# Kernel optimization log

Hardware: AMD Instinct MI355X
Metric: run time of the kernel (lower is better)

## Reference

```python
import jax, jax.numpy as jnp
import numpy as np

IMAGE_SIZE = 800
OUT = 50          # feature map size
FEAT = 512
SCALES = (2.0, 4.0, 6.0)
RATIOS = (0.5, 1.0, 1.5)
A = len(SCALES) * len(RATIOS)          # 9 anchors per cell
POS_THR, NEG_THR = 0.7, 0.3
W_CONF, W_REG = 1.0, 5.0
SCALE = IMAGE_SIZE // OUT              # 16, stride of feature map


def _anchor_base():
    # order: ratio outer loop, scale inner loop (matches get_anchor_base)
    ws = jnp.array([s * r for r in RATIOS for s in SCALES], jnp.float32)  # [A]
    hs = jnp.array([s for r in RATIOS for s in SCALES], jnp.float32)      # [A]
    cx = (jnp.arange(OUT, dtype=jnp.float32) + 0.5)[:, None, None]        # grid dim0 -> x
    cy = (jnp.arange(OUT, dtype=jnp.float32) + 0.5)[None, :, None]        # grid dim1 -> y
    xmin = jnp.clip(cx - ws / 2, 0.0, OUT)
    xmax = jnp.clip(cx + ws / 2, 0.0, OUT)
    ymin = jnp.clip(cy - hs / 2, 0.0, OUT)
    ymax = jnp.clip(cy + hs / 2, 0.0, OUT)
    shp = (OUT, OUT, A)
    base = jnp.stack([jnp.broadcast_to(xmin, shp), jnp.broadcast_to(ymin, shp),
                      jnp.broadcast_to(xmax, shp), jnp.broadcast_to(ymax, shp)], axis=-1)
    return base.reshape(-1, 4)         # [N,4], N = OUT*OUT*A = 22500


def _iou(anchors, gt):
    # anchors [N,4], gt [B,M,4] (xyxy) -> iou [B,N,M]
    a = anchors[None, :, None, :]
    g = gt[:, None, :, :]
    ix1 = jnp.maximum(a[..., 0], g[..., 0]); iy1 = jnp.maximum(a[..., 1], g[..., 1])
    ix2 = jnp.minimum(a[..., 2], g[..., 2]); iy2 = jnp.minimum(a[..., 3], g[..., 3])
    inter = jnp.clip(ix2 - ix1, 0.0) * jnp.clip(iy2 - iy1, 0.0)
    area_a = (a[..., 2] - a[..., 0]) * (a[..., 3] - a[..., 1])
    area_g = (g[..., 2] - g[..., 0]) * (g[..., 3] - g[..., 1])
    return inter / (area_a + area_g - inter + 1e-8)


def _smooth_l1(d):
    ad = jnp.abs(d)
    return jnp.where(ad < 1.0, 0.5 * d * d, ad - 0.5)


def setup_inputs() -> dict:
    key = jax.random.key(0)
    ks = jax.random.split(key, 8)
    B, M = 16, 16
    features = jax.random.normal(ks[0], (B, FEAT, OUT, OUT), jnp.float32)
    # valid GT boxes in image coords: centers in [100,700], sizes in [32,200]
    cxy = jax.random.uniform(ks[1], (B, M, 2), jnp.float32, 100.0, 700.0)
    wh = jax.random.uniform(ks[2], (B, M, 2), jnp.float32, 32.0, 200.0)
    x1y1 = jnp.clip(cxy - wh / 2, 0.0, IMAGE_SIZE)
    x2y2 = jnp.clip(cxy + wh / 2, 0.0, IMAGE_SIZE)
    gt_boxes = jnp.concatenate([x1y1, x2y2], axis=-1)
    w1 = jax.random.normal(ks[3], (FEAT, FEAT, 3, 3), jnp.float32) * 0.02
    b1 = jnp.zeros((FEAT,), jnp.float32)
    w_cls = jax.random.normal(ks[4], (A, FEAT), jnp.float32) * 0.02
    b_cls = jnp.zeros((A,), jnp.float32)
    w_box = jax.random.normal(ks[5], (4 * A, FEAT), jnp.float32) * 0.02
    b_box = jnp.zeros((4 * A,), jnp.float32)
    return {"features": features, "gt_boxes": gt_boxes, "w1": w1, "b1": b1,
            "w_cls": w_cls, "b_cls": b_cls, "w_box": w_box, "b_box": b_box}


def reference(features, gt_boxes, w1, b1, w_cls, b_cls, w_box, b_box):
    B = features.shape[0]
    anchors = _anchor_base()                                   # [N,4]
    N = anchors.shape[0]

    # --- conv tower ---
    x = jax.lax.conv_general_dilated(features, w1, (1, 1), 'SAME') + b1[None, :, None, None]
    cls_map = jnp.einsum('bchw,ac->bahw', x, w_cls) + b_cls[None, :, None, None]   # [B,A,H,W]
    box_map = jnp.einsum('bchw,dc->bdhw', x, w_box) + b_box[None, :, None, None]   # [B,4A,H,W]
    logits = jnp.transpose(cls_map, (0, 2, 3, 1)).reshape(B, N)                    # [B,N]
    pred_off = jnp.transpose(box_map.reshape(B, A, 4, OUT, OUT), (0, 3, 4, 1, 2)).reshape(B, N, 4)

    # --- project gt to feature-map (anchor) coords, 'p2a' ---
    gt = gt_boxes / SCALE                                       # [B,M,4]

    # --- anchor/GT assignment ---
    iou = _iou(anchors, gt)                                     # [B,N,M]
    max_per_gt = jnp.max(iou, axis=1, keepdims=True)            # best anchor per gt
    pos_mask = ((iou == max_per_gt) & (max_per_gt > 0)) | (iou > POS_THR)  # [B,N,M]
    pos_mask = pos_mask.astype(jnp.float32)
    n_pos = jnp.maximum(pos_mask.sum(), 1.0)

    # --- gt offsets (standard tx,ty,tw,th) for every (anchor,gt) pair ---
    acx = (anchors[:, 0] + anchors[:, 2]) / 2
    acy = (anchors[:, 1] + anchors[:, 3]) / 2
    aw = jnp.maximum(anchors[:, 2] - anchors[:, 0], 1e-6)
    ah = jnp.maximum(anchors[:, 3] - anchors[:, 1], 1e-6)
    gcx = (gt[..., 0] + gt[..., 2]) / 2                         # [B,M]
    gcy = (gt[..., 1] + gt[..., 3]) / 2
    gw = jnp.maximum(gt[..., 2] - gt[..., 0], 1e-6)
    gh = jnp.maximum(gt[..., 3] - gt[..., 1], 1e-6)
    tx = (gcx[:, None, :] - acx[None, :, None]) / aw[None, :, None]   # [B,N,M]
    ty = (gcy[:, None, :] - acy[None, :, None]) / ah[None, :, None]
    tw = jnp.log(gw[:, None, :] / aw[None, :, None])
    th = jnp.log(gh[:, None, :] / ah[None, :, None])
    gt_off = jnp.stack([tx, ty, tw, th], axis=-1)               # [B,N,M,4]

    diff = gt_off - pred_off[:, :, None, :]
    reg_loss = (pos_mask[..., None] * _smooth_l1(diff)).sum() / (4.0 * n_pos)

    # --- classification loss: BCE-with-logits; positives=1, negatives=0 ---
    pos_loss = (pos_mask * jax.nn.softplus(-logits)[:, :, None]).sum() / n_pos
    neg_anchor = jnp.all(iou < NEG_THR, axis=2).astype(jnp.float32)   # [B,N]
    n_neg = jnp.maximum(neg_anchor.sum(), 1.0)
    neg_loss = (neg_anchor * jax.nn.softplus(logits)).sum() / n_neg
    cls_loss = 0.5 * (pos_loss + neg_loss)

    total_rpn_loss = W_CONF * cls_loss + W_REG * reg_loss

    # --- proposals from predicted offsets for all anchors ---
    pcx = acx[None, :] + pred_off[..., 0] * aw[None, :]
    pcy = acy[None, :] + pred_off[..., 1] * ah[None, :]
    pw = aw[None, :] * jnp.exp(pred_off[..., 2])
    ph = ah[None, :] * jnp.exp(pred_off[..., 3])
    proposals = jnp.stack([pcx - pw / 2, pcy - ph / 2, pcx + pw / 2, pcy + ph / 2], axis=-1)  # [B,N,4]

    return total_rpn_loss, proposals
```

## Files before the change

### kernel.cpp

```cpp
#include <hip/hip_runtime.h>
#include <hip/hip_bf16.h>
#include <stdint.h>

using bf16x8 = __attribute__((ext_vector_type(8))) __bf16;
using f32x4  = __attribute__((ext_vector_type(4))) float;

#define FT_POS_B 1280
#define W2_CHUNK_B 34560

__device__ __forceinline__ unsigned short f2bf(float f) {
  union { float f; unsigned u; } x; x.f = f;
  unsigned r = x.u + 0x7fffu + ((x.u >> 16) & 1u);
  return (unsigned short)(r >> 16);
}

__device__ __forceinline__ void gl_lds16(const void* g, void* l) {
  __builtin_amdgcn_global_load_lds(
      (const __attribute__((address_space(1))) void*)g,
      (__attribute__((address_space(3))) void*)l, 16, 0, 0);
}

__device__ __forceinline__ float sl1(float d) {
  float ad = fabsf(d);
  return ad < 1.f ? 0.5f * d * d : ad - 0.5f;
}
__device__ __forceinline__ float softplus_f(float x) {
  return fmaxf(x, 0.f) + log1pf(expf(-fabsf(x)));
}

__device__ __forceinline__ void anchor_strict(int n, float& ax1, float& ay1,
                                              float& ax2, float& ay2) {
  int ii = n / 450;
  int rem = n - ii * 450;
  int jj = rem / 9;
  int a  = rem - jj * 9;
  const float SC[3] = {2.f, 4.f, 6.f};
  const float RA[3] = {0.5f, 1.f, 1.5f};
  float w = __fmul_rn(SC[a % 3], RA[a / 3]);
  float h = SC[a % 3];
  float cx = __fadd_rn((float)ii, 0.5f);
  float cy = __fadd_rn((float)jj, 0.5f);
  float wh = __fmul_rn(w, 0.5f), hh = __fmul_rn(h, 0.5f);
  ax1 = fminf(fmaxf(__fsub_rn(cx, wh), 0.f), 50.f);
  ax2 = fminf(fmaxf(__fadd_rn(cx, wh), 0.f), 50.f);
  ay1 = fminf(fmaxf(__fsub_rn(cy, hh), 0.f), 50.f);
  ay2 = fminf(fmaxf(__fadd_rn(cy, hh), 0.f), 50.f);
}
__device__ __forceinline__ float iou_strict(float ax1, float ay1, float ax2, float ay2,
                                            float aarea, const float* __restrict__ g) {
  float gx1 = __fmul_rn(g[0], 0.0625f), gy1 = __fmul_rn(g[1], 0.0625f);
  float gx2 = __fmul_rn(g[2], 0.0625f), gy2 = __fmul_rn(g[3], 0.0625f);
  float ix1 = fmaxf(ax1, gx1), iy1 = fmaxf(ay1, gy1);
  float ix2 = fminf(ax2, gx2), iy2 = fminf(ay2, gy2);
  float inter = __fmul_rn(fmaxf(__fsub_rn(ix2, ix1), 0.f),
                          fmaxf(__fsub_rn(iy2, iy1), 0.f));
  float garea = __fmul_rn(__fsub_rn(gx2, gx1), __fsub_rn(gy2, gy1));
  float denom = __fadd_rn(__fsub_rn(__fadd_rn(aarea, garea), inter), 1e-8f);
  return __fdiv_rn(inter, denom);
}

__global__ __launch_bounds__(256) void k_featT(const float* __restrict__ feat,
                                               char* __restrict__ featT2) {
  int row = blockIdx.x;
  int cq  = blockIdx.y;
  int b = row / 50, i = row - b * 50;
  int w = threadIdx.x >> 6, lane = threadIdx.x & 63;
  if (lane >= 50) return;
  size_t rbase = (size_t)b * 1280000 + (size_t)i * 50 + lane;
  char* wpos = featT2 + (size_t)((b * 52 + i + 1) * 52 + (lane + 1)) * FT_POS_B;
#pragma unroll
  for (int k = 0; k < 2; ++k) {
    int c0 = cq * 64 + w * 8 + k * 32;
    __align__(16) unsigned short tmp[8];
#pragma unroll
    for (int t = 0; t < 8; ++t) tmp[t] = f2bf(feat[rbase + (size_t)(c0 + t) * 2500]);
    *(uint4*)(wpos + (c0 >> 5) * 80 + (c0 & 31) * 2) = *(const uint4*)tmp;
  }
}

__global__ __launch_bounds__(128) void k_weff1(const float* __restrict__ w1,
                                               const float* __restrict__ wc,
                                               const float* __restrict__ wb,
                                               float* __restrict__ part) {
  __shared__ float sW[48][64];
  const int t = threadIdx.x;
  const int kmem = blockIdx.x * 128 + t;
  const int cz = blockIdx.y;
#pragma unroll
  for (int q = 0; q < 24; ++q) {
    int idx = t + q * 128;
    int co = idx >> 6, cl = idx & 63;
    int c = cz * 64 + cl;
    float v = 0.f;
    if (co < 9) v = wc[co * 512 + c];
    else if (co < 45) v = wb[(co - 9) * 512 + c];
    sW[co][cl] = v;
  }
  __syncthreads();
  float acc[48];
#pragma unroll
  for (int co = 0; co < 48; ++co) acc[co] = 0.f;
  const float* w1p = w1 + (size_t)(cz * 64) * 4608 + kmem;
  for (int c4 = 0; c4 < 64; c4 += 4) {
    float f0 = w1p[(size_t)(c4 + 0) * 4608];
    float f1 = w1p[(size_t)(c4 + 1) * 4608];
    float f2 = w1p[(size_t)(c4 + 2) * 4608];
    float f3 = w1p[(size_t)(c4 + 3) * 4608];
#pragma unroll
    for (int co = 0; co < 48; ++co) {
      float4 wv = *(const float4*)&sW[co][c4];
      acc[co] += wv.x * f0 + wv.y * f1 + wv.z * f2 + wv.w * f3;
    }
  }
  float* dst = part + (size_t)cz * 221184 + kmem;
#pragma unroll
  for (int co = 0; co < 48; ++co) dst[(size_t)co * 4608] = acc[co];
}

__global__ __launch_bounds__(256) void k_weff2(const float* __restrict__ part,
                                               unsigned short* __restrict__ w2) {
  int idx = blockIdx.x * 256 + threadIdx.x;
  int c = idx / 17280;  int r = idx - c * 17280;
  int tap = r / 1920;   int r2 = r - tap * 1920;
  int co = r2 / 40;     int e = r2 - co * 40;
  float s = 0.f;
  if (e < 32) {
    int ci = c * 32 + e;
    const float* p = part + (size_t)co * 4608 + ci * 9 + tap;
#pragma unroll
    for (int cz = 0; cz < 8; ++cz) s += p[(size_t)cz * 221184];
  }
  w2[idx] = f2bf(s);
}

__global__ __launch_bounds__(64) void k_bias(const float* __restrict__ wc,
                                             const float* __restrict__ wb,
                                             const float* __restrict__ b1,
                                             const float* __restrict__ bc,
                                             const float* __restrict__ bbx,
                                             float* __restrict__ bias_eff) {
  int co = blockIdx.x, l = threadIdx.x;
  float s = 0.f;
#pragma unroll
  for (int q = 0; q < 8; ++q) {
    int c = q * 64 + l;
    float wv = co < 9 ? wc[co * 512 + c] : (co < 45 ? wb[(co - 9) * 512 + c] : 0.f);
    s += wv * b1[c];
  }
  for (int o = 32; o; o >>= 1) s += __shfl_down(s, o, 64);
  if (l == 0)
    bias_eff[co] = s + (co < 9 ? bc[co] : (co < 45 ? bbx[co - 9] : 0.f));
}

__global__ __launch_bounds__(256) void k_iou(const float* __restrict__ gt_boxes,
                                             unsigned* __restrict__ mx) {
  int b = blockIdx.y;
  int n = blockIdx.x * 256 + threadIdx.x;
  float lm[16];
#pragma unroll
  for (int m = 0; m < 16; ++m) lm[m] = 0.f;
  if (n < 22500) {
    float ax1, ay1, ax2, ay2;
    anchor_strict(n, ax1, ay1, ax2, ay2);
    float aarea = __fmul_rn(__fsub_rn(ax2, ax1), __fsub_rn(ay2, ay1));
#pragma unroll
    for (int m = 0; m < 16; ++m)
      lm[m] = iou_strict(ax1, ay1, ax2, ay2, aarea, gt_boxes + (b * 16 + m) * 4);
  }
  __shared__ float red[4][16];
#pragma unroll
  for (int m = 0; m < 16; ++m) {
    float v = lm[m];
    for (int o = 32; o; o >>= 1) v = fmaxf(v, __shfl_down(v, o, 64));
    if ((threadIdx.x & 63) == 0) red[threadIdx.x >> 6][m] = v;
  }
  __syncthreads();
  if (threadIdx.x < 16) {
    float v = fmaxf(fmaxf(red[0][threadIdx.x], red[1][threadIdx.x]),
                    fmaxf(red[2][threadIdx.x], red[3][threadIdx.x]));
    atomicMax(mx + b * 16 + threadIdx.x, __float_as_uint(v));
  }
}

__global__ __launch_bounds__(256) void k_conv(const char* __restrict__ featT2,
                                              const char* __restrict__ w2,
                                              const float* __restrict__ beff,
                                              float* __restrict__ oh) {
  __shared__ __align__(16) char sF[2][19456];
  __shared__ __align__(16) char sA[2][34816];
  const int tid = threadIdx.x, lane = tid & 63, w = tid >> 6;
  const int bx = blockIdx.x;
  const int b = bx >> 4, tl = bx & 15, tr = tl >> 2, tc = tl & 3;
  const int i0 = tr * 13 - (tr == 3 ? 1 : 0);
  const int TI = (tr >= 2) ? 12 : 13;
  const int j0 = tc * 13 - (tc == 3 ? 1 : 0);
  const int TJ = (tc >= 2) ? 12 : 13;
  const int TJ2 = TJ + 2;
  const int mcount = TI * TJ;
  const int pieces = (TI + 2) * TJ2 * 5;

  const char* srcF[5];
#pragma unroll
  for (int k = 0; k < 5; ++k) {
    int s = w * 5 + k;
    int pi = s * 64 + lane;
    if (pi >= pieces) pi = pieces - 1;
    int pos = pi / 5, pc = pi - pos * 5;
    int hi = pos / TJ2, hj = pos - hi * TJ2;
    srcF[k] = featT2 + (size_t)((b * 52 + i0 + hi) * 52 + (j0 + hj)) * FT_POS_B + pc * 16;
  }
  int idxB[3];
#pragma unroll
  for (int bf = 0; bf < 3; ++bf) {
    int p = (w * 3 + bf) * 16 + (lane & 15);
    if (p >= mcount) p = mcount - 1;
    int di = p / TJ, dj = p - di * TJ;
    idxB[bf] = (di * TJ2 + dj) * 80 + (lane >> 4) * 16;
  }
  const int aoff = (lane & 15) * 80 + (lane >> 4) * 16;
  int toff[9];
#pragma unroll
  for (int tp = 0; tp < 9; ++tp) toff[tp] = ((tp / 3) * TJ2 + (tp % 3)) * 80;

  f32x4 acc[3][3] = {};

  auto stage = [&](int c, int pb) {
#pragma unroll
    for (int k = 0; k < 5; ++k) {
      int s = w * 5 + k;
      if (s < 18) gl_lds16(srcF[k] + (size_t)c * 80, sF[pb] + s * 1024);
    }
#pragma unroll
    for (int k = 0; k < 9; ++k) {
      int s = w + 4 * k;
      if (s < 34)
        gl_lds16(w2 + (size_t)c * W2_CHUNK_B + s * 1024 + lane * 16, sA[pb] + s * 1024);
    }
  };

  stage(0, 0);
  __builtin_amdgcn_s_waitcnt(0);
  __syncthreads();

  for (int c = 0; c < 16; ++c) {
    int pb = c & 1;
    if (c < 15) stage(c + 1, pb ^ 1);
    const char* fA = sA[pb];
    const char* fB = sF[pb];
#pragma unroll
    for (int tp = 0; tp < 9; ++tp) {
      bf16x8 av[3], bv[3];
#pragma unroll
      for (int cf = 0; cf < 3; ++cf)
        av[cf] = *(const bf16x8*)(fA + tp * 3840 + cf * 1280 + aoff);
#pragma unroll
      for (int bf = 0; bf < 3; ++bf)
        bv[bf] = *(const bf16x8*)(fB + idxB[bf] + toff[tp]);
#pragma unroll
      for (int cf = 0; cf < 3; ++cf)
#pragma unroll
        for (int bf = 0; bf < 3; ++bf)
          acc[cf][bf] = __builtin_amdgcn_mfma_f32_16x16x32_bf16(av[cf], bv[bf], acc[cf][bf], 0, 0, 0);
    }
    __builtin_amdgcn_s_waitcnt(0);
    __syncthreads();
  }

  f32x4 bias[3];
#pragma unroll
  for (int cf = 0; cf < 3; ++cf)
    bias[cf] = *(const f32x4*)(beff + cf * 16 + (lane >> 4) * 4);
#pragma unroll
  for (int bf = 0; bf < 3; ++bf) {
    int p = (w * 3 + bf) * 16 + (lane & 15);
    if (p >= mcount) continue;
    int di = p / TJ, dj = p - di * TJ;
    int gm = (b * 50 + i0 + di) * 50 + (j0 + dj);
#pragma unroll
    for (int cf = 0; cf < 3; ++cf) {
      f32x4 v = acc[cf][bf];
#pragma unroll
      for (int r = 0; r < 4; ++r) v[r] += bias[cf][r];
      *(f32x4*)(oh + (size_t)gm * 48 + cf * 16 + (lane >> 4) * 4) = v;
    }
  }
}

__global__ __launch_bounds__(256) void k_loss(const float* __restrict__ gt_boxes,
                                              const unsigned* __restrict__ mxbuf,
                                              const float* __restrict__ oh,
                                              float* __restrict__ accum,
                                              float* __restrict__ dout) {
  int b = blockIdx.y;
  int n = blockIdx.x * 256 + threadIdx.x;
  float s_np = 0.f, s_reg = 0.f, s_pos = 0.f, s_nc = 0.f, s_nl = 0.f;
  if (n < 22500) {
    float ax1, ay1, ax2, ay2;
    anchor_strict(n, ax1, ay1, ax2, ay2);
    float aarea = __fmul_rn(__fsub_rn(ax2, ax1), __fsub_rn(ay2, ay1));
    float acx = (ax1 + ax2) * 0.5f, acy = (ay1 + ay2) * 0.5f;
    float aw = fmaxf(ax2 - ax1, 1e-6f), ah = fmaxf(ay2 - ay1, 1e-6f);
    int ii = n / 450, rem = n - ii * 450, jj = rem / 9, a = rem - jj * 9;
    const float* row = oh + ((size_t)(b * 2500 + ii * 50 + jj)) * 48;
    float logit = row[a];
    float p0 = row[9 + a * 4], p1 = row[10 + a * 4];
    float p2 = row[11 + a * 4], p3 = row[12 + a * 4];
    int npos = 0;
    bool allneg = true;
#pragma unroll
    for (int m = 0; m < 16; ++m) {
      const float* g = gt_boxes + (b * 16 + m) * 4;
      float iou = iou_strict(ax1, ay1, ax2, ay2, aarea, g);
      float mxv = __uint_as_float(mxbuf[b * 16 + m]);
      bool pos = ((iou == mxv) && (mxv > 0.f)) || (iou > 0.7f);
      if (iou >= 0.3f) allneg = false;
      if (pos) {
        ++npos;
        float gx1 = g[0] * 0.0625f, gy1 = g[1] * 0.0625f;
        float gx2 = g[2] * 0.0625f, gy2 = g[3] * 0.0625f;
        float gcx = (gx1 + gx2) * 0.5f, gcy = (gy1 + gy2) * 0.5f;
        float gw = fmaxf(gx2 - gx1, 1e-6f), gh = fmaxf(gy2 - gy1, 1e-6f);
        float tx = (gcx - acx) / aw, ty = (gcy - acy) / ah;
        float twv = logf(gw / aw), thv = logf(gh / ah);
        s_reg += sl1(tx - p0) + sl1(ty - p1) + sl1(twv - p2) + sl1(thv - p3);
      }
    }
    s_np = (float)npos;
    s_pos = (float)npos * softplus_f(-logit);
    if (allneg) { s_nc = 1.f; s_nl = softplus_f(logit); }
    float pcx = acx + p0 * aw, pcy = acy + p1 * ah;
    float pw = aw * expf(p2), ph = ah * expf(p3);
    float* o = dout + 1 + ((size_t)b * 22500 + n) * 4;
    o[0] = pcx - pw * 0.5f;
    o[1] = pcy - ph * 0.5f;
    o[2] = pcx + pw * 0.5f;
    o[3] = pcy + ph * 0.5f;
  }
  float vals[5] = {s_np, s_reg, s_pos, s_nc, s_nl};
  __shared__ float red[4][5];
#pragma unroll
  for (int q = 0; q < 5; ++q) {
    float v = vals[q];
    for (int o = 32; o; o >>= 1) v += __shfl_down(v, o, 64);
    if ((threadIdx.x & 63) == 0) red[threadIdx.x >> 6][q] = v;
  }
  __syncthreads();
  if (threadIdx.x < 5) {
    float v = red[0][threadIdx.x] + red[1][threadIdx.x] +
              red[2][threadIdx.x] + red[3][threadIdx.x];
    atomicAdd(accum + threadIdx.x, v);
  }
}

__global__ void k_fin(const float* __restrict__ accum, float* __restrict__ dout) {
  if (threadIdx.x == 0 && blockIdx.x == 0) {
    float np = fmaxf(accum[0], 1.f);
    float nn = fmaxf(accum[3], 1.f);
    float loss = 0.5f * (accum[2] / np + accum[4] / nn) + 5.f * (accum[1] / (4.f * np));
    dout[0] = loss;
  }
}

extern "C" void kernel_launch(void* const* d_in, const int* in_sizes, int n_in,
                              void* d_out, int out_size, void* d_ws, size_t ws_size,
                              hipStream_t stream) {
  const float* features = (const float*)d_in[0];
  const float* gt_boxes = (const float*)d_in[1];
  const float* w1    = (const float*)d_in[2];
  const float* b1    = (const float*)d_in[3];
  const float* w_cls = (const float*)d_in[4];
  const float* b_cls = (const float*)d_in[5];
  const float* w_box = (const float*)d_in[6];
  const float* b_box = (const float*)d_in[7];
  float* out = (float*)d_out;
  char* ws = (char*)d_ws;

  char*           featT2 = ws;
  unsigned short* w2     = (unsigned short*)(ws + 55377920);
  float*          wpart  = (float*)(ws + 55930880);
  float*          oh     = (float*)(ws + 63008768);
  float*          beff   = (float*)(ws + 70688768);
  unsigned*       mx     = (unsigned*)(ws + 70688960);
  float*          accum  = (float*)(ws + 70689984);

  hipMemsetAsync(featT2, 0, 55377920, stream);
  hipMemsetAsync(ws + 70688960, 0, 1056, stream);

  k_featT<<<dim3(800, 8), 256, 0, stream>>>(features, featT2);
  k_weff1<<<dim3(36, 8), 128, 0, stream>>>(w1, w_cls, w_box, wpart);
  k_weff2<<<1080, 256, 0, stream>>>(wpart, w2);
  k_bias<<<48, 64, 0, stream>>>(w_cls, w_box, b1, b_cls, b_box, beff);
  k_iou<<<dim3(88, 16), 256, 0, stream>>>(gt_boxes, mx);
  k_conv<<<256, 256, 0, stream>>>(featT2, (const char*)w2, beff, oh);
  k_loss<<<dim3(88, 16), 256, 0, stream>>>(gt_boxes, mx, oh, accum, out);
  k_fin<<<1, 64, 0, stream>>>(accum, out);
}
```

Before: 296.9 us.

## Transpose features through LDS and zero only halo borders instead of memsetting

The feature transpose kernel now stages a 64-position by 256-channel tile in shared memory. It uses coalesced float4 loads along the spatial axis and writes each position's channel records as 16-byte vector stores. The full 55 MB memset of the padded buffer is removed; a dedicated tile index zeroes only the halo border positions. This cuts a large redundant write pass and improves read coalescing. In exchange, the 16 pad bytes inside each 80-byte record are no longer zeroed, which is only safe if the conv kernel never reads them.

```diff
diff --git a/kernel.cpp b/kernel.cpp
--- a/kernel.cpp
+++ b/kernel.cpp
@@ -61,20 +61,66 @@
 
 __global__ __launch_bounds__(256) void k_featT(const float* __restrict__ feat,
                                                char* __restrict__ featT2) {
-  int row = blockIdx.x;
-  int cq  = blockIdx.y;
-  int b = row / 50, i = row - b * 50;
-  int w = threadIdx.x >> 6, lane = threadIdx.x & 63;
-  if (lane >= 50) return;
-  size_t rbase = (size_t)b * 1280000 + (size_t)i * 50 + lane;
-  char* wpos = featT2 + (size_t)((b * 52 + i + 1) * 52 + (lane + 1)) * FT_POS_B;
-#pragma unroll
-  for (int k = 0; k < 2; ++k) {
-    int c0 = cq * 64 + w * 8 + k * 32;
-    __align__(16) unsigned short tmp[8];
-#pragma unroll
-    for (int t = 0; t < 8; ++t) tmp[t] = f2bf(feat[rbase + (size_t)(c0 + t) * 2500]);
-    *(uint4*)(wpos + (c0 >> 5) * 80 + (c0 & 31) * 2) = *(const uint4*)tmp;
+  const int tile = blockIdx.x;
+  const int h    = blockIdx.y;
+  const int b    = blockIdx.z;
+  const int tid  = threadIdx.x;
+  if (tile == 40) {
+    uint4 z = {0, 0, 0, 0};
+    for (int u = tid; u < 204 * 8; u += 256) {
+      int p = u >> 3, rec = u & 7;
+      int ip, jp;
+      if (p < 52)       { ip = 0;       jp = p; }
+      else if (p < 104) { ip = 51;      jp = p - 52; }
+      else if (p < 154) { ip = p - 103; jp = 0; }
+      else              { ip = p - 153; jp = 51; }
+      char* dst = featT2 + (size_t)((b * 52 + ip) * 52 + jp) * FT_POS_B
+                + (h * 8 + rec) * 80;
+      *(uint4*)(dst)      = z;
+      *(uint4*)(dst + 16) = z;
+      *(uint4*)(dst + 32) = z;
+      *(uint4*)(dst + 48) = z;
+    }
+    return;
+  }
+  __shared__ __align__(16) unsigned short sT[64][264];
+  const int pos0 = tile * 64;
+  const float* fb = feat + (size_t)b * 1280000 + (size_t)h * 256 * 2500;
+  const int psub = (tid & 15) * 4;
+#pragma unroll 4
+  for (int it = 0; it < 16; ++it) {
+    int ci = it * 16 + (tid >> 4);
+    int p = pos0 + psub;
+    float4 v;
+    if (p + 3 < 2500) {
+      v = *(const float4*)(fb + (size_t)ci * 2500 + p);
+    } else {
+      v.x = fb[(size_t)ci * 2500 + min(p + 0, 2499)];
+      v.y = fb[(size_t)ci * 2500 + min(p + 1, 2499)];
+      v.z = fb[(size_t)ci * 2500 + min(p + 2, 2499)];
+      v.w = fb[(size_t)ci * 2500 + min(p + 3, 2499)];
+    }
+    sT[psub + 0][ci] = f2bf(v.x);
+    sT[psub + 1][ci] = f2bf(v.y);
+    sT[psub + 2][ci] = f2bf(v.z);
+    sT[psub + 3][ci] = f2bf(v.w);
+  }
+  __syncthreads();
+#pragma unroll
+  for (int q = 0; q < 2; ++q) {
+    int u = tid + q * 256;
+    int p = u >> 3, rec = u & 7;
+    int gp = pos0 + p;
+    if (gp >= 2500) continue;
+    int i = gp / 50, j = gp - i * 50;
+    char* dst = featT2 + (size_t)((b * 52 + i + 1) * 52 + (j + 1)) * FT_POS_B
+              + (h * 8 + rec) * 80;
+    const uint4* src = (const uint4*)&sT[p][rec * 32];
+    uint4 a0 = src[0], a1 = src[1], a2 = src[2], a3 = src[3];
+    *(uint4*)(dst)      = a0;
+    *(uint4*)(dst + 16) = a1;
+    *(uint4*)(dst + 32) = a2;
+    *(uint4*)(dst + 48) = a3;
   }
 }
 
@@ -383,10 +429,9 @@
   unsigned*       mx     = (unsigned*)(ws + 70688960);
   float*          accum  = (float*)(ws + 70689984);
 
-  hipMemsetAsync(featT2, 0, 55377920, stream);
   hipMemsetAsync(ws + 70688960, 0, 1056, stream);
 
-  k_featT<<<dim3(800, 8), 256, 0, stream>>>(features, featT2);
+  k_featT<<<dim3(41, 2, 16), 256, 0, stream>>>(features, featT2);
   k_weff1<<<dim3(36, 8), 128, 0, stream>>>(w1, w_cls, w_box, wpart);
   k_weff2<<<1080, 256, 0, stream>>>(wpart, w2);
   k_bias<<<48, 64, 0, stream>>>(w_cls, w_box, b1, b_cls, b_box, beff);
```

After: 279.9 us. 1.06x faster.
